# Performance work log

Hardware: AMD Instinct MI355X
Metric: run time of the kernel (lower is better)

The kernel has to match this reference:

```python
import jax, jax.numpy as jnp
import numpy as np

B, L, H, C = 32, 2048, 512, 50
KERNEL = 3  # avgpool kernel, stride 1, pad 1, count_include_pad=False


def _avgpool3_no_pad_count(x):
    """AvgPool1d(kernel=3, stride=1, pad=1, count_include_pad=False) along last axis.
    x: (..., L). Zero-pad, sum 3-tap windows, divide by number of valid elements."""
    pad = [(0, 0)] * (x.ndim - 1) + [(1, 1)]
    xp = jnp.pad(x, pad)
    s = xp[..., :-2] + xp[..., 1:-1] + xp[..., 2:]
    ones = jnp.pad(jnp.ones_like(x), pad)
    cnt = ones[..., :-2] + ones[..., 1:-1] + ones[..., 2:]
    return s / cnt


def setup_inputs() -> dict:
    key = jax.random.key(0)
    k1, k2, k3, k4, k5, k6 = jax.random.split(key, 6)
    sent_keys = jax.random.normal(k1, (B, L, H), dtype=jnp.float32)
    sent_values = jax.random.normal(k2, (B, L, H), dtype=jnp.float32)
    sent_lens = jax.random.randint(k3, (B,), 1, L + 1).astype(jnp.int64)
    W1 = jax.random.normal(k4, (H, H), dtype=jnp.float32) * 0.02
    W2 = jax.random.normal(k5, (H, H), dtype=jnp.float32) * 0.02
    W3 = jax.random.normal(k6, (C, H), dtype=jnp.float32) * 0.02
    return {"sent_keys": sent_keys, "sent_values": sent_values,
            "sent_lens": sent_lens, "W1": W1, "W2": W2, "W3": W3}


def reference(sent_keys, sent_values, sent_lens, W1, W2, W3):
    # Tiny MLP scorer (dropout is identity in eval mode)
    p1 = jnp.tanh(jnp.einsum('blh,kh->blk', sent_keys, W1))   # (B,L,H)
    p2 = jnp.tanh(jnp.einsum('blh,kh->blk', p1, W2))          # (B,L,H)
    p3 = jnp.einsum('blh,ch->blc', p1 + p2, W3)               # (B,L,C)

    b, l, c = p3.shape
    # Fill padded positions with the score at the last valid position (index len-1)
    last_idx = (sent_lens - 1).astype(jnp.int32)[:, None, None]        # (B,1,1)
    last = jnp.take_along_axis(p3, jnp.broadcast_to(last_idx, (b, 1, c)), axis=1)  # (B,1,C)
    mask = (jnp.arange(l)[None, :] < sent_lens[:, None])[:, :, None]   # (B,L,1)
    kq = jnp.where(mask, p3, last)

    # Smooth along doc-position axis with avgpool(count_include_pad=False)
    smoothened_kq = _avgpool3_no_pad_count(kq.transpose(0, 2, 1)).transpose(0, 2, 1)  # (B,L,C)

    # Softmax over classes, then zero out padded positions
    attention_values = jax.nn.softmax(smoothened_kq, axis=2)
    attention_values = jnp.where(mask, attention_values, 0.0)

    # (B,C,L) @ (B,L,H) -> (B,C,H)
    class_inputs = jnp.einsum('blc,blh->bch', attention_values, sent_values)
    return attention_values, class_inputs, smoothened_kq
```

## Files before the change

### kernel.cpp

```cpp
#include <hip/hip_runtime.h>
#include <cstdint>

#define Bc 32
#define Lc 2048
#define Hc 512
#define Cc 50
#define Mc (Bc*Lc)

typedef short s8v   __attribute__((ext_vector_type(8)));
typedef float f4v   __attribute__((ext_vector_type(4)));

__device__ inline unsigned short f2bf(float f) {
    unsigned int u = __float_as_uint(f);
    u += 0x7fffu + ((u >> 16) & 1u);
    return (unsigned short)(u >> 16);
}
__device__ inline float bf2f(unsigned short h) {
    return __uint_as_float(((unsigned int)h) << 16);
}
__device__ inline void gl_lds16(const unsigned short* g, unsigned short* l) {
    __builtin_amdgcn_global_load_lds(
        (const __attribute__((address_space(1))) unsigned int*)g,
        (__attribute__((address_space(3))) unsigned int*)l, 16, 0, 0);
}

__global__ __launch_bounds__(256)
void f32_to_bf16_kernel(const float* __restrict__ in, unsigned short* __restrict__ out)
{
    size_t i = ((size_t)blockIdx.x * 256 + threadIdx.x) * 8;
    float4 a = *(const float4*)(in + i);
    float4 b = *(const float4*)(in + i + 4);
    s8v o;
    o[0]=f2bf(a.x); o[1]=f2bf(a.y); o[2]=f2bf(a.z); o[3]=f2bf(a.w);
    o[4]=f2bf(b.x); o[5]=f2bf(b.y); o[6]=f2bf(b.z); o[7]=f2bf(b.w);
    *(s8v*)(out + i) = o;
}

__global__ __launch_bounds__(256)
void convert_weights_kernel(const float* __restrict__ W1, const float* __restrict__ W2,
                            const float* __restrict__ W3,
                            unsigned short* __restrict__ W1b,
                            unsigned short* __restrict__ W2b,
                            unsigned short* __restrict__ W3b)
{
    int e = (blockIdx.x * 256 + threadIdx.x) * 8;
    if (e >= 524288) {
        int off = e - 524288;
        int row = off >> 9;
        s8v o;
        #pragma unroll
        for (int j = 0; j < 8; ++j)
            o[j] = (row < Cc) ? (short)f2bf(W3[off + j]) : (short)0;
        *(s8v*)(W3b + off) = o;
        return;
    }
    const float* src = (e < 262144) ? W1 : W2;
    unsigned short* dst = (e < 262144) ? W1b : W2b;
    int off = (e < 262144) ? e : e - 262144;
    float4 a = *(const float4*)(src + off);
    float4 b = *(const float4*)(src + off + 4);
    s8v o;
    o[0]=f2bf(a.x); o[1]=f2bf(a.y); o[2]=f2bf(a.z); o[3]=f2bf(a.w);
    o[4]=f2bf(b.x); o[5]=f2bf(b.y); o[6]=f2bf(b.z); o[7]=f2bf(b.w);
    *(s8v*)(dst + off) = o;
}

__global__ __launch_bounds__(256)
void transpose_v_kernel(const float* __restrict__ V, unsigned short* __restrict__ Vt)
{
    __shared__ float tile[64 * 65];
    const int l0 = blockIdx.x * 64;
    const int h0 = blockIdx.y * 64;
    const int b  = blockIdx.z;
    const int tid = threadIdx.x;
    const int li = tid >> 2;
    const int hq = (tid & 3) * 4;

    const float* src = V + ((size_t)(b * Lc + l0 + li)) * Hc + h0 + hq;
    #pragma unroll
    for (int j = 0; j < 4; ++j) {
        float4 v = *(const float4*)(src + 16 * j);
        float* d = &tile[li * 65 + hq + 16 * j];
        d[0] = v.x; d[1] = v.y; d[2] = v.z; d[3] = v.w;
    }
    __syncthreads();

    const int lane = tid & 63;
    const int w    = tid >> 6;
    #pragma unroll
    for (int i = 0; i < 16; ++i) {
        int hr = i * 4 + w;
        unsigned short* dst = Vt + ((size_t)(b * Hc + h0 + hr)) * Lc + l0 + lane;
        *dst = f2bf(tile[lane * 65 + hr]);
    }
}

__global__ __launch_bounds__(256)
void mfma_gemm512(const unsigned short* __restrict__ Ab,
                  const unsigned short* __restrict__ Wb,
                  unsigned short* __restrict__ Ob, int mode)
{
    __shared__ alignas(16) unsigned short As[128 * 32];
    __shared__ alignas(16) unsigned short Bs[128 * 32];
    const int tid = threadIdx.x;
    const int w = tid >> 6, l = tid & 63;
    const int j0 = blockIdx.x * 128;
    const int i0 = blockIdx.y * 128;

    const int sr  = w * 16 + (l >> 2);
    const int kg8 = (l & 3) * 8;
    const unsigned short* Ag0 = Ab + (size_t)(i0 + sr) * 512 + kg8;
    const unsigned short* Ag1 = Ag0 + (size_t)64 * 512;
    const unsigned short* Bg0 = Wb + (size_t)(j0 + sr) * 512 + kg8;
    const unsigned short* Bg1 = Bg0 + (size_t)64 * 512;
    unsigned short* Al0 = As + w * 512;
    unsigned short* Al1 = As + 2048 + w * 512;
    unsigned short* Bl0 = Bs + w * 512;
    unsigned short* Bl1 = Bs + 2048 + w * 512;

    const int wm = (w & 1) * 64, wn = (w >> 1) * 64;
    const int fr = l & 15;
    const int fq = (l >> 4) * 8;

    f4v acc[4][4];
    #pragma unroll
    for (int r = 0; r < 4; ++r)
        #pragma unroll
        for (int c = 0; c < 4; ++c) acc[r][c] = (f4v){0.f, 0.f, 0.f, 0.f};

    for (int k0 = 0; k0 < 512; k0 += 32) {
        gl_lds16(Ag0 + k0, Al0);
        gl_lds16(Ag1 + k0, Al1);
        gl_lds16(Bg0 + k0, Bl0);
        gl_lds16(Bg1 + k0, Bl1);
        __syncthreads();
        s8v af[4], bf[4];
        #pragma unroll
        for (int r = 0; r < 4; ++r)
            af[r] = *(const s8v*)&As[(wm + r * 16 + fr) * 32 + fq];
        #pragma unroll
        for (int c = 0; c < 4; ++c)
            bf[c] = *(const s8v*)&Bs[(wn + c * 16 + fr) * 32 + fq];
        #pragma unroll
        for (int r = 0; r < 4; ++r)
            #pragma unroll
            for (int c = 0; c < 4; ++c)
                acc[r][c] = __builtin_amdgcn_mfma_f32_16x16x32_bf16(
                    af[r], bf[c], acc[r][c], 0, 0, 0);
        __syncthreads();
    }

    #pragma unroll
    for (int r = 0; r < 4; ++r)
        #pragma unroll
        for (int v = 0; v < 4; ++v) {
            const int row = i0 + wm + r * 16 + (l >> 4) * 4 + v;
            #pragma unroll
            for (int c = 0; c < 4; ++c) {
                const int col = j0 + wn + c * 16 + fr;
                float x = tanhf(acc[r][c][v]);
                if (mode) x += bf2f(Ab[(size_t)row * 512 + col]);
                Ob[(size_t)row * 512 + col] = f2bf(x);
            }
        }
}

__global__ __launch_bounds__(256)
void mfma_gemm_p3(const unsigned short* __restrict__ Sb,
                  const unsigned short* __restrict__ W3b,
                  float* __restrict__ P3)
{
    __shared__ alignas(16) unsigned short As[128 * 32];
    __shared__ alignas(16) unsigned short Bs[64 * 32];
    const int tid = threadIdx.x;
    const int w = tid >> 6, l = tid & 63;
    const int i0 = blockIdx.x * 128;

    const int sr  = w * 16 + (l >> 2);
    const int kg8 = (l & 3) * 8;
    const unsigned short* Ag0 = Sb + (size_t)(i0 + sr) * 512 + kg8;
    const unsigned short* Ag1 = Ag0 + (size_t)64 * 512;
    const unsigned short* Bg  = W3b + (size_t)sr * 512 + kg8;
    unsigned short* Al0 = As + w * 512;
    unsigned short* Al1 = As + 2048 + w * 512;
    unsigned short* Bl  = Bs + w * 512;

    const int wm = w * 32;
    const int fr = l & 15;
    const int fq = (l >> 4) * 8;

    f4v acc[2][4];
    #pragma unroll
    for (int r = 0; r < 2; ++r)
        #pragma unroll
        for (int c = 0; c < 4; ++c) acc[r][c] = (f4v){0.f, 0.f, 0.f, 0.f};

    for (int k0 = 0; k0 < 512; k0 += 32) {
        gl_lds16(Ag0 + k0, Al0);
        gl_lds16(Ag1 + k0, Al1);
        gl_lds16(Bg + k0, Bl);
        __syncthreads();
        s8v af[2], bf[4];
        #pragma unroll
        for (int r = 0; r < 2; ++r)
            af[r] = *(const s8v*)&As[(wm + r * 16 + fr) * 32 + fq];
        #pragma unroll
        for (int c = 0; c < 4; ++c)
            bf[c] = *(const s8v*)&Bs[(c * 16 + fr) * 32 + fq];
        #pragma unroll
        for (int r = 0; r < 2; ++r)
            #pragma unroll
            for (int c = 0; c < 4; ++c)
                acc[r][c] = __builtin_amdgcn_mfma_f32_16x16x32_bf16(
                    af[r], bf[c], acc[r][c], 0, 0, 0);
        __syncthreads();
    }

    #pragma unroll
    for (int r = 0; r < 2; ++r)
        #pragma unroll
        for (int v = 0; v < 4; ++v) {
            const int row = i0 + wm + r * 16 + (l >> 4) * 4 + v;
            #pragma unroll
            for (int c = 0; c < 4; ++c) {
                const int col = c * 16 + fr;
                if (col < Cc) P3[(size_t)row * Cc + col] = acc[r][c][v];
            }
        }
}

__global__ __launch_bounds__(64)
void normalize_lens_kernel(const int* __restrict__ raw, int* __restrict__ lens)
{
    __shared__ int is64;
    if (threadIdx.x == 0) {
        int orv = 0;
        for (int i = 1; i < 32; i += 2) orv |= raw[i];
        is64 = (orv == 0) ? 1 : 0;
    }
    __syncthreads();
    int b = threadIdx.x;
    if (b < Bc) lens[b] = is64 ? raw[2*b] : raw[b];
}

__global__ __launch_bounds__(256)
void pool_softmax_kernel(const float* __restrict__ P3, const int* __restrict__ lens,
                         float* __restrict__ out_attn, float* __restrict__ out_smooth,
                         unsigned short* __restrict__ attnT)
{
    const int idx = blockIdx.x * 256 + threadIdx.x;
    const int b = idx >> 11;
    const int l = idx & (Lc - 1);
    const int len = lens[b];
    const float* base = P3 + (size_t)b * Lc * Cc;

    const int  r0 = min(l, len - 1);
    const bool hm = (l > 0);
    const bool hp = (l < Lc - 1);
    const int  rm = hm ? min(l - 1, len - 1) : 0;
    const int  rp = hp ? min(l + 1, len - 1) : 0;
    const float cnt = 1.f + (hm ? 1.f : 0.f) + (hp ? 1.f : 0.f);

    float sm[Cc];
    float mx = -1e30f;
    #pragma unroll
    for (int c = 0; c < Cc; ++c) {
        float s = base[(size_t)r0 * Cc + c];
        if (hm) s += base[(size_t)rm * Cc + c];
        if (hp) s += base[(size_t)rp * Cc + c];
        s = s / cnt;
        sm[c] = s;
        mx = fmaxf(mx, s);
    }
    float* srow = out_smooth + (size_t)idx * Cc;
    #pragma unroll
    for (int c = 0; c < Cc; ++c) srow[c] = sm[c];

    float sum = 0.f;
    #pragma unroll
    for (int c = 0; c < Cc; ++c) {
        float e = __expf(sm[c] - mx);
        sm[c] = e;
        sum += e;
    }
    const float inv = 1.f / sum;
    const bool valid = (l < len);
    float* arow = out_attn + (size_t)idx * Cc;
    unsigned short* trow = attnT + (size_t)b * 64 * Lc + l;
    #pragma unroll
    for (int c = 0; c < Cc; ++c) {
        float a = valid ? sm[c] * inv : 0.f;
        arow[c] = a;
        trow[(size_t)c * Lc] = f2bf(a);
    }
}

__global__ __launch_bounds__(256)
void class_mfma_kernel(const unsigned short* __restrict__ attnT,
                       const unsigned short* __restrict__ Vt,
                       float* __restrict__ out_class)
{
    __shared__ alignas(16) unsigned short As[64 * 32];
    __shared__ alignas(16) unsigned short Bs[128 * 32];
    const int tid = threadIdx.x;
    const int w = tid >> 6, l = tid & 63;
    const int n0 = blockIdx.x * 128;
    const int b  = blockIdx.y;
    const int kb = blockIdx.z * 512;

    const int sr  = w * 16 + (l >> 2);
    const int kg8 = (l & 3) * 8;
    const unsigned short* Ag  = attnT + ((size_t)b * 64 + sr) * Lc + kg8;
    const unsigned short* Bg0 = Vt + ((size_t)(b * Hc + n0 + sr)) * Lc + kg8;
    const unsigned short* Bg1 = Bg0 + (size_t)64 * Lc;
    unsigned short* Al  = As + w * 512;
    unsigned short* Bl0 = Bs + w * 512;
    unsigned short* Bl1 = Bs + 2048 + w * 512;

    const int fr = l & 15;
    const int fq = (l >> 4) * 8;

    f4v acc[4][2];
    #pragma unroll
    for (int r = 0; r < 4; ++r)
        #pragma unroll
        for (int c = 0; c < 2; ++c) acc[r][c] = (f4v){0.f, 0.f, 0.f, 0.f};

    for (int k0 = kb; k0 < kb + 512; k0 += 32) {
        gl_lds16(Ag + k0, Al);
        gl_lds16(Bg0 + k0, Bl0);
        gl_lds16(Bg1 + k0, Bl1);
        __syncthreads();
        s8v af[4], bf[2];
        #pragma unroll
        for (int r = 0; r < 4; ++r)
            af[r] = *(const s8v*)&As[(r * 16 + fr) * 32 + fq];
        #pragma unroll
        for (int c = 0; c < 2; ++c)
            bf[c] = *(const s8v*)&Bs[(w * 32 + c * 16 + fr) * 32 + fq];
        #pragma unroll
        for (int r = 0; r < 4; ++r)
            #pragma unroll
            for (int c = 0; c < 2; ++c)
                acc[r][c] = __builtin_amdgcn_mfma_f32_16x16x32_bf16(
                    af[r], bf[c], acc[r][c], 0, 0, 0);
        __syncthreads();
    }

    #pragma unroll
    for (int r = 0; r < 4; ++r)
        #pragma unroll
        for (int v = 0; v < 4; ++v) {
            const int m = r * 16 + (l >> 4) * 4 + v;
            if (m < Cc) {
                #pragma unroll
                for (int c = 0; c < 2; ++c) {
                    const int h = n0 + w * 32 + c * 16 + fr;
                    atomicAdd(out_class + ((size_t)b * Cc + m) * Hc + h,
                              acc[r][c][v]);
                }
            }
        }
}

extern "C" void kernel_launch(void* const* d_in, const int* in_sizes, int n_in,
                              void* d_out, int out_size, void* d_ws, size_t ws_size,
                              hipStream_t stream)
{
    const float* keys     = (const float*)d_in[0];
    const float* vals     = (const float*)d_in[1];
    const int*   lens_raw = (const int*)d_in[2];
    const float* W1       = (const float*)d_in[3];
    const float* W2       = (const float*)d_in[4];
    const float* W3       = (const float*)d_in[5];

    char* ws = (char*)d_ws;
    const size_t MB = 1024 * 1024;
    unsigned short* Akv  = (unsigned short*)ws;
    float*          P3   = (float*)ws;
    unsigned short* P1b  = (unsigned short*)(ws + 64 * MB);
    unsigned short* Vt   = (unsigned short*)(ws + 64 * MB);
    unsigned short* Sb   = (unsigned short*)(ws + 128 * MB);
    unsigned short* W1b  = (unsigned short*)(ws + 192 * MB);
    unsigned short* W2b  = W1b + Hc * Hc;
    unsigned short* W3b  = W2b + Hc * Hc;
    unsigned short* attnT= (unsigned short*)(ws + 194 * MB);
    int*            lens = (int*)(ws + 202 * MB);

    float* out_attn   = (float*)d_out;
    float* out_class  = out_attn + (size_t)Bc * Lc * Cc;
    float* out_smooth = out_class + (size_t)Bc * Cc * Hc;

    hipMemsetAsync(out_class, 0, (size_t)Bc * Cc * Hc * sizeof(float), stream);

    f32_to_bf16_kernel<<<(Mc * Hc / 8) / 256, 256, 0, stream>>>(keys, Akv);
    convert_weights_kernel<<<272, 256, 0, stream>>>(W1, W2, W3, W1b, W2b, W3b);
    normalize_lens_kernel<<<1, 64, 0, stream>>>(lens_raw, lens);

    mfma_gemm512<<<dim3(4, Mc / 128), 256, 0, stream>>>(Akv, W1b, P1b, 0);
    mfma_gemm512<<<dim3(4, Mc / 128), 256, 0, stream>>>(P1b, W2b, Sb, 1);
    transpose_v_kernel<<<dim3(Lc / 64, Hc / 64, Bc), 256, 0, stream>>>(vals, Vt);
    mfma_gemm_p3<<<Mc / 128, 256, 0, stream>>>(Sb, W3b, P3);
    pool_softmax_kernel<<<Mc / 256, 256, 0, stream>>>(P3, lens, out_attn, out_smooth, attnT);
    class_mfma_kernel<<<dim3(4, Bc, 4), 256, 0, stream>>>(attnT, Vt, out_class);
}
```

Before: 545.1 us.

## Use fast exp-based tanh, pad P3 rows to 52, vectorize pool-softmax I/O

```diff
diff --git a/kernel.cpp b/kernel.cpp
--- a/kernel.cpp
+++ b/kernel.cpp
@@ -5,6 +5,7 @@
 #define Lc 2048
 #define Hc 512
 #define Cc 50
+#define PCc 52
 #define Mc (Bc*Lc)
 
 typedef short s8v   __attribute__((ext_vector_type(8)));
@@ -17,6 +18,10 @@
 }
 __device__ inline float bf2f(unsigned short h) {
     return __uint_as_float(((unsigned int)h) << 16);
+}
+__device__ inline float fast_tanh(float x) {
+    float e = __expf(2.0f * x);
+    return 1.0f - 2.0f / (e + 1.0f);
 }
 __device__ inline void gl_lds16(const unsigned short* g, unsigned short* l) {
     __builtin_amdgcn_global_load_lds(
@@ -158,7 +163,7 @@
             #pragma unroll
             for (int c = 0; c < 4; ++c) {
                 const int col = j0 + wn + c * 16 + fr;
-                float x = tanhf(acc[r][c][v]);
+                float x = fast_tanh(acc[r][c][v]);
                 if (mode) x += bf2f(Ab[(size_t)row * 512 + col]);
                 Ob[(size_t)row * 512 + col] = f2bf(x);
             }
@@ -224,7 +229,7 @@
             #pragma unroll
             for (int c = 0; c < 4; ++c) {
                 const int col = c * 16 + fr;
-                if (col < Cc) P3[(size_t)row * Cc + col] = acc[r][c][v];
+                if (col < Cc) P3[(size_t)row * PCc + col] = acc[r][c][v];
             }
         }
 }
@@ -252,29 +257,51 @@
     const int b = idx >> 11;
     const int l = idx & (Lc - 1);
     const int len = lens[b];
-    const float* base = P3 + (size_t)b * Lc * Cc;
+    const float* base = P3 + (size_t)b * Lc * PCc;
 
     const int  r0 = min(l, len - 1);
     const bool hm = (l > 0);
     const bool hp = (l < Lc - 1);
     const int  rm = hm ? min(l - 1, len - 1) : 0;
     const int  rp = hp ? min(l + 1, len - 1) : 0;
-    const float cnt = 1.f + (hm ? 1.f : 0.f) + (hp ? 1.f : 0.f);
-
-    float sm[Cc];
+    const float rcnt = 1.f / (1.f + (hm ? 1.f : 0.f) + (hp ? 1.f : 0.f));
+
+    float sm[PCc];
+    const float* p0 = base + (size_t)r0 * PCc;
+    #pragma unroll
+    for (int q = 0; q < 13; ++q) {
+        f4v v = *(const f4v*)(p0 + q * 4);
+        sm[q*4+0] = v[0]; sm[q*4+1] = v[1]; sm[q*4+2] = v[2]; sm[q*4+3] = v[3];
+    }
+    if (hm) {
+        const float* p = base + (size_t)rm * PCc;
+        #pragma unroll
+        for (int q = 0; q < 13; ++q) {
+            f4v v = *(const f4v*)(p + q * 4);
+            sm[q*4+0] += v[0]; sm[q*4+1] += v[1]; sm[q*4+2] += v[2]; sm[q*4+3] += v[3];
+        }
+    }
+    if (hp) {
+        const float* p = base + (size_t)rp * PCc;
+        #pragma unroll
+        for (int q = 0; q < 13; ++q) {
+            f4v v = *(const f4v*)(p + q * 4);
+            sm[q*4+0] += v[0]; sm[q*4+1] += v[1]; sm[q*4+2] += v[2]; sm[q*4+3] += v[3];
+        }
+    }
+
     float mx = -1e30f;
     #pragma unroll
     for (int c = 0; c < Cc; ++c) {
-        float s = base[(size_t)r0 * Cc + c];
-        if (hm) s += base[(size_t)rm * Cc + c];
-        if (hp) s += base[(size_t)rp * Cc + c];
-        s = s / cnt;
-        sm[c] = s;
-        mx = fmaxf(mx, s);
+        sm[c] *= rcnt;
+        mx = fmaxf(mx, sm[c]);
     }
     float* srow = out_smooth + (size_t)idx * Cc;
     #pragma unroll
-    for (int c = 0; c < Cc; ++c) srow[c] = sm[c];
+    for (int q = 0; q < 25; ++q) {
+        float2 v = make_float2(sm[q*2], sm[q*2+1]);
+        *(float2*)(srow + q * 2) = v;
+    }
 
     float sum = 0.f;
     #pragma unroll
@@ -285,14 +312,17 @@
     }
     const float inv = 1.f / sum;
     const bool valid = (l < len);
+    const float scale = valid ? inv : 0.f;
     float* arow = out_attn + (size_t)idx * Cc;
     unsigned short* trow = attnT + (size_t)b * 64 * Lc + l;
     #pragma unroll
-    for (int c = 0; c < Cc; ++c) {
-        float a = valid ? sm[c] * inv : 0.f;
-        arow[c] = a;
-        trow[(size_t)c * Lc] = f2bf(a);
-    }
+    for (int c = 0; c < Cc; ++c) sm[c] *= scale;
+    #pragma unroll
+    for (int q = 0; q < 25; ++q)
+        *(float2*)(arow + q * 2) = make_float2(sm[q*2], sm[q*2+1]);
+    #pragma unroll
+    for (int c = 0; c < Cc; ++c)
+        trow[(size_t)c * Lc] = f2bf(sm[c]);
 }
 
 __global__ __launch_bounds__(256)
```

New measurement: 524.1 us. 3.8% less time.
